# Optimization experiments

Measured on AMD Instinct MI355X. Metric: run time of the kernel, lower is better.

The kernel has to match this reference:

```python
import jax, jax.numpy as jnp
import numpy as np

N_LAYERS = 4
D_MODEL = 256
P = 128            # ssm_size // 2 (conj_sym S5)
LATENT_DIM = 256
MAX_SEQ_LEN = 32768
OUTPUT_DIM = 64
LN_EPS = 1e-6      # flax nn.LayerNorm default


def layer_norm(x, scale, bias):
    mu = jnp.mean(x, axis=-1, keepdims=True)
    var = jnp.mean(jnp.square(x - mu), axis=-1, keepdims=True)
    return (x - mu) * jax.lax.rsqrt(var + LN_EPS) * scale + bias


def s5_ssm(u, Lre, Lim, Bre, Bim, Cre, Cim, Dvec, log_step, resets):
    """u: (L, H) float. Returns (L, H) float. conj_sym S5, zoh discretization."""
    step = jnp.exp(log_step)                       # (P,)
    Lam = Lre + 1j * Lim                           # (P,) complex
    Lam_bar = jnp.exp(Lam * step)                  # (P,)
    B_bar = ((Lam_bar - 1.0) / Lam)[:, None] * (Bre + 1j * Bim)  # (P, H)
    Bu = u @ B_bar.T                               # (L, P) complex
    A = jnp.broadcast_to(Lam_bar, Bu.shape)        # (L, P)
    c = resets[:, None].astype(u.dtype)            # (L, 1)

    def binop(qi, qj):
        Ai, bi, ci = qi
        Aj, bj, cj = qj
        return (Aj * Ai * (1.0 - cj) + Aj * cj,
                (Aj * bi + bj) * (1.0 - cj) + bj * cj,
                ci * (1.0 - cj) + cj)

    # zero initial hidden state => no prepend needed (identical result)
    _, xs, _ = jax.lax.associative_scan(binop, (A, Bu, c))
    y = 2.0 * jnp.real(xs @ (Cre + 1j * Cim).T)    # (L, H), conj_sym doubling
    return y + u * Dvec


def setup_inputs() -> dict:
    key = jax.random.key(0)
    ks = jax.random.split(key, 16)
    f = jax.random.normal
    return {
        "latent": f(ks[0], (LATENT_DIM,), jnp.float32),
        "W_expand": f(ks[1], (LATENT_DIM, D_MODEL), jnp.float32) / np.sqrt(LATENT_DIM),
        "b_expand": jnp.zeros((D_MODEL,), jnp.float32),
        "norm_scale": jnp.ones((N_LAYERS, D_MODEL), jnp.float32),
        "norm_bias": jnp.zeros((N_LAYERS, D_MODEL), jnp.float32),
        "Lambda_re": -(0.1 + 0.9 * jax.random.uniform(ks[2], (N_LAYERS, P))),
        "Lambda_im": np.pi * f(ks[3], (N_LAYERS, P), jnp.float32),
        "B_re": f(ks[4], (N_LAYERS, P, D_MODEL), jnp.float32) / np.sqrt(D_MODEL),
        "B_im": f(ks[5], (N_LAYERS, P, D_MODEL), jnp.float32) / np.sqrt(D_MODEL),
        "C_re": f(ks[6], (N_LAYERS, D_MODEL, P), jnp.float32) / np.sqrt(P),
        "C_im": f(ks[7], (N_LAYERS, D_MODEL, P), jnp.float32) / np.sqrt(P),
        "D": f(ks[8], (N_LAYERS, D_MODEL), jnp.float32),
        "log_step": jnp.log(jax.random.uniform(ks[9], (N_LAYERS, P), minval=1e-3, maxval=1e-1)),
        "W1": f(ks[10], (N_LAYERS, D_MODEL, D_MODEL), jnp.float32) / np.sqrt(D_MODEL),
        "b1": jnp.zeros((N_LAYERS, D_MODEL), jnp.float32),
        "W2": f(ks[11], (N_LAYERS, D_MODEL, D_MODEL), jnp.float32) / np.sqrt(D_MODEL),
        "b2": jnp.zeros((N_LAYERS, D_MODEL), jnp.float32),
        "W_out": f(ks[12], (D_MODEL, OUTPUT_DIM), jnp.float32) / np.sqrt(D_MODEL),
        "b_out": jnp.zeros((OUTPUT_DIM,), jnp.float32),
        "seq_len": MAX_SEQ_LEN,
    }


def reference(latent, W_expand, b_expand, norm_scale, norm_bias,
              Lambda_re, Lambda_im, B_re, B_im, C_re, C_im, D, log_step,
              W1, b1, W2, b2, W_out, b_out, seq_len):
    # latent_expand + leaky_relu, then broadcast to full trajectory
    x = jax.nn.leaky_relu(latent @ W_expand + b_expand)        # (H,)
    x = jnp.broadcast_to(x[None, :], (MAX_SEQ_LEN, D_MODEL))    # (L, H); batch dim of 1 dropped
    resets = jnp.zeros((MAX_SEQ_LEN,), x.dtype)                 # dones = zeros
    for i in range(N_LAYERS):
        skip = x
        h = layer_norm(x, norm_scale[i], norm_bias[i])          # prenorm
        y = s5_ssm(h, Lambda_re[i], Lambda_im[i], B_re[i], B_im[i],
                   C_re[i], C_im[i], D[i], log_step[i], resets)
        y = layer_norm(y, norm_scale[i], norm_bias[i])          # gtrxl norm (shared params)
        y = jax.nn.gelu(y)
        y = (y @ W1[i] + b1[i]) * jax.nn.sigmoid(y @ W2[i] + b2[i])  # full_glu
        x = skip + y
    return x @ W_out + b_out                                    # (L, output_dim)
```

## Files before the change

### kernel.cpp

```cpp
#include <hip/hip_runtime.h>
#include <stdint.h>

#define LSEQ 32768
#define NCH 512
#define TCH 64

typedef _Float16 half8 __attribute__((ext_vector_type(8)));
typedef _Float16 half4v __attribute__((ext_vector_type(4)));
typedef _Float16 half2v __attribute__((ext_vector_type(2)));
typedef float f32x4 __attribute__((ext_vector_type(4)));
typedef float f32x2 __attribute__((ext_vector_type(2)));

__device__ __forceinline__ float sigmoidf_(float x) { return 1.f / (1.f + __expf(-x)); }
__device__ __forceinline__ float gelu_(float x) {
    float z = 0.7978845608028654f * (x + 0.044715f * x * x * x);
    float e = __expf(2.f * z);
    float t = 1.f - 2.f / (e + 1.f);
    return 0.5f * x * (1.f + t);
}

__device__ __forceinline__ void gll16(const _Float16* gp, _Float16* lp) {
    __builtin_amdgcn_global_load_lds((__attribute__((address_space(1))) void*)gp,
                                     (__attribute__((address_space(3))) void*)lp, 16, 0, 0);
}

__global__ __launch_bounds__(512) void s5_k0a(const float* __restrict__ lre, const float* __restrict__ lim,
                                              const float* __restrict__ lstep,
                                              float* aR, float* aI, float* cbR, float* cbI,
                                              float* aTR, float* aTI, float* alp, float* ralp) {
    int i = threadIdx.x;
    float st = expf(lstep[i]);
    float lr = lre[i] * st, li = lim[i] * st;
    float ea = expf(lr);
    float ar = ea * cosf(li), ai = ea * sinf(li);
    float den = lre[i] * lre[i] + lim[i] * lim[i];
    float nr = ar - 1.f, ni = ai;
    float cr = (nr * lre[i] + ni * lim[i]) / den;
    float ci = (ni * lre[i] - nr * lim[i]) / den;
    float cm = sqrtf(cr * cr + ci * ci);
    float al = sqrtf(2.83f / fmaxf(cm, 1e-8f));
    float eT = expf(lr * (float)TCH);
    aR[i] = ar; aI[i] = ai;
    cbR[i] = cr; cbI[i] = ci;
    aTR[i] = eT * cosf(li * (float)TCH);
    aTI[i] = eT * sinf(li * (float)TCH);
    alp[i] = al; ralp[i] = 1.f / al;
}

__global__ __launch_bounds__(256) void s5_k0b(const float* __restrict__ Bre, const float* __restrict__ Bim,
                                              const float* __restrict__ Cre, const float* __restrict__ Cim,
                                              const float* __restrict__ W1, const float* __restrict__ W2,
                                              const float* __restrict__ b1, const float* __restrict__ b2,
                                              const float* __restrict__ Wout,
                                              const float* __restrict__ cbR, const float* __restrict__ cbI,
                                              const float* __restrict__ alp, const float* __restrict__ ralp,
                                              _Float16* Wbu, _Float16* Wc, _Float16* Wglu,
                                              _Float16* WoutT, float* bglu) {
    int stride = gridDim.x * blockDim.x;
    int tid0 = blockIdx.x * blockDim.x + threadIdx.x;
    for (int i = tid0; i < 262144; i += stride) {
        int l = i >> 16, n = (i >> 8) & 255, k = i & 255;
        int s = n >> 4, lmn = n & 15;
        int p = l * 128 + (s >> 1) * 16 + lmn;
        float re = cbR[p] * Bre[p * 256 + k] - cbI[p] * Bim[p * 256 + k];
        float im = cbR[p] * Bim[p * 256 + k] + cbI[p] * Bre[p * 256 + k];
        Wbu[i] = (_Float16)(((s & 1) ? im : re) * alp[p]);
    }
    for (int i = tid0; i < 262144; i += stride) {
        int l = i >> 16, n = (i >> 8) & 255, k = i & 255;
        int p = k >> 1;
        float base = (k & 1) ? -2.f * Cim[(l * 256 + n) * 128 + p]
                             : 2.f * Cre[(l * 256 + n) * 128 + p];
        Wc[i] = (_Float16)(base * ralp[l * 128 + p]);
    }
    for (int i = tid0; i < 524288; i += stride) {
        int l = i >> 17, n = (i >> 8) & 511, k = i & 255;
        int j = ((n >> 7) << 6) | (((n >> 6) & 1) << 5) | (((n >> 5) & 1) << 4) | (n & 15);
        const float* src = ((n >> 4) & 1) ? W2 : W1;
        Wglu[i] = (_Float16)src[(l * 256 + k) * 256 + j];
    }
    for (int i = tid0; i < 16384; i += stride) {
        int n = i >> 8, k = i & 255;
        WoutT[i] = (_Float16)Wout[k * 64 + n];
    }
    for (int i = tid0; i < 2048; i += stride) {
        int l = i >> 9, n = i & 511;
        int j = ((n >> 7) << 6) | (((n >> 6) & 1) << 5) | (((n >> 5) & 1) << 4) | (n & 15);
        bglu[i] = (((n >> 4) & 1) ? b2 : b1)[l * 256 + j];
    }
}

__global__ __launch_bounds__(256) void s5_k0c(const float* __restrict__ latent, const float* __restrict__ W,
                                              const float* __restrict__ b, _Float16* __restrict__ x0h) {
    __shared__ float lat[256];
    lat[threadIdx.x] = latent[threadIdx.x];
    __syncthreads();
    float s = b[threadIdx.x];
    for (int k = 0; k < 256; ++k) s += lat[k] * W[k * 256 + threadIdx.x];
    x0h[threadIdx.x] = (_Float16)((s > 0.f) ? s : 0.01f * s);
}

__global__ __launch_bounds__(256) void s5_k1_fill(const _Float16* __restrict__ x0h, _Float16* __restrict__ x) {
    int i = blockIdx.x * 256 + threadIdx.x;
    half8 v = *(const half8*)(x0h + (i & 31) * 8);
    *(half8*)(x + i * 8) = v;
}

__global__ __launch_bounds__(512, 1) void s5_k3_lngemm(const _Float16* __restrict__ x,
                                                       const _Float16* __restrict__ Wt,
                                                       const float* __restrict__ gamma,
                                                       const float* __restrict__ beta,
                                                       _Float16* __restrict__ h,
                                                       _Float16* __restrict__ Buh) {
    __shared__ _Float16 sW[128 * 512];
    int tid = threadIdx.x, wid = tid >> 6, lane = tid & 63;
    int lm = lane & 15, quad = lane >> 4;
    int m0 = blockIdx.x * 128;
    int rowb = m0 + wid * 16;

#pragma unroll
    for (int half = 0; half < 2; ++half)
#pragma unroll
        for (int i = 0; i < 8; ++i) {
            int c = i * 8 + wid;
            int ks = c >> 3, n16 = c & 7;
            gll16(Wt + (half * 128 + n16 * 16 + lm) * 256 + ks * 32 + quad * 8,
                  sW + half * 32768 + c * 512);
        }

    int row = rowb + lm;
    half8 af[8];
    {
        half8 xv[8];
#pragma unroll
        for (int ks = 0; ks < 8; ++ks)
            xv[ks] = *(const half8*)(x + row * 256 + ks * 32 + quad * 8);
        float s1 = 0.f, s2 = 0.f;
#pragma unroll
        for (int i = 0; i < 8; ++i)
#pragma unroll
            for (int j = 0; j < 8; ++j) { float t = (float)xv[i][j]; s1 += t; s2 += t * t; }
        s1 += __shfl_xor(s1, 16, 64); s2 += __shfl_xor(s2, 16, 64);
        s1 += __shfl_xor(s1, 32, 64); s2 += __shfl_xor(s2, 32, 64);
        float mu = s1 * (1.f / 256.f);
        float var = s2 * (1.f / 256.f) - mu * mu;
        float rs = rsqrtf(fmaxf(var, 0.f) + 1e-6f);
#pragma unroll
        for (int ks = 0; ks < 8; ++ks) {
            f32x4 g0 = *(const f32x4*)(gamma + ks * 32 + quad * 8);
            f32x4 g1 = *(const f32x4*)(gamma + ks * 32 + quad * 8 + 4);
            f32x4 b0 = *(const f32x4*)(beta + ks * 32 + quad * 8);
            f32x4 b1 = *(const f32x4*)(beta + ks * 32 + quad * 8 + 4);
            half8 o;
#pragma unroll
            for (int j = 0; j < 4; ++j) {
                o[j]     = (_Float16)(((float)xv[ks][j] - mu) * rs * g0[j] + b0[j]);
                o[j + 4] = (_Float16)(((float)xv[ks][j + 4] - mu) * rs * g1[j] + b1[j]);
            }
            af[ks] = o;
            *(half8*)(h + row * 256 + ks * 32 + quad * 8) = o;
        }
    }
    asm volatile("s_waitcnt vmcnt(0)" ::: "memory");
    __syncthreads();

    f32x4 zero = {0.f, 0.f, 0.f, 0.f};
    f32x4 acc[2][8];
#pragma unroll
    for (int hf = 0; hf < 2; ++hf)
#pragma unroll
        for (int nt = 0; nt < 8; ++nt) acc[hf][nt] = zero;

#pragma unroll
    for (int hf = 0; hf < 2; ++hf)
#pragma unroll
        for (int ks = 0; ks < 8; ++ks) {
            half8 bf[8];
#pragma unroll
            for (int nt = 0; nt < 8; ++nt)
                bf[nt] = *(const half8*)(sW + hf * 32768 + (ks * 8 + nt) * 512 + lane * 8);
#pragma unroll
            for (int nt = 0; nt < 8; ++nt)
                acc[hf][nt] = __builtin_amdgcn_mfma_f32_16x16x32_f16(af[ks], bf[nt], acc[hf][nt], 0, 0, 0);
        }

#pragma unroll
    for (int u = 0; u < 8; ++u) {
        int hf = u >> 2, q = u & 3;
        int p = u * 16 + lm;
#pragma unroll
        for (int r = 0; r < 4; ++r) {
            half2v o = {(_Float16)acc[hf][2 * q][r], (_Float16)acc[hf][2 * q + 1][r]};
            *(half2v*)(Buh + (rowb + quad * 4 + r) * 256 + 2 * p) = o;
        }
    }
}

__global__ __launch_bounds__(128, 4) void s5_k4_carry(const _Float16* __restrict__ Bu,
                                                      const float* __restrict__ aR, const float* __restrict__ aI,
                                                      float* __restrict__ carRI) {
    int p = threadIdx.x, c = blockIdx.x;
    int t0 = c * TCH;
    const _Float16* bp = Bu + t0 * 256 + 2 * p;
    half2v hv[TCH];
#pragma unroll
    for (int j = 0; j < TCH; ++j) hv[j] = *(const half2v*)(bp + j * 256);
    float ar = aR[p], ai = aI[p];
    float sr = 0.f, si = 0.f;
#pragma unroll
    for (int j = 0; j < TCH; ++j) {
        float nr = fmaf(ar, sr, fmaf(-ai, si, (float)hv[j][0]));
        float ni = fmaf(ar, si, fmaf(ai, sr, (float)hv[j][1]));
        sr = nr; si = ni;
    }
    *(f32x2*)(carRI + (c * 128 + p) * 2) = f32x2{sr, si};
}

__global__ __launch_bounds__(512, 1) void s5_k7_gemm_c(const _Float16* __restrict__ Bu,
                                                       const float* __restrict__ carRI,
                                                       const _Float16* __restrict__ Wt,
                                                       const _Float16* __restrict__ h,
                                                       const float* __restrict__ aR, const float* __restrict__ aI,
                                                       const float* __restrict__ aTR, const float* __restrict__ aTI,
                                                       const float* __restrict__ Dv,
                                                       const float* __restrict__ gamma,
                                                       const float* __restrict__ beta,
                                                       _Float16* __restrict__ g) {
    __shared__ _Float16 sW[64 * 512];
    __shared__ _Float16 xsT[128 * 256];
    int tid = threadIdx.x, wid = tid >> 6, lane = tid & 63;
    int lm = lane & 15, quad = lane >> 4;
    int m0 = blockIdx.x * 128;
    int rowb = m0 + wid * 16;

    auto stageW = [&](int half) {
#pragma unroll
        for (int i = 0; i < 8; ++i) {
            int c = i * 8 + wid;
            int ks = c >> 3, n16 = c & 7;
            gll16(Wt + (half * 128 + n16 * 16 + lm) * 256 + ks * 32 + quad * 8, sW + c * 512);
        }
    };
    stageW(0);

    if (tid < 256) {
        int cc = tid >> 7, p = tid & 127;
        int cg = blockIdx.x * 2 + cc;
        const _Float16* bp = Bu + (m0 + cc * TCH) * 256 + 2 * p;
        half2v hv[TCH];
#pragma unroll
        for (int j = 0; j < TCH; ++j) hv[j] = *(const half2v*)(bp + j * 256);
        float tr = aTR[p], ti = aTI[p];
        float cr = 0.f, ci = 0.f;
#pragma unroll 8
        for (int i = 0; i < cg; ++i) {
            f32x2 w = *(const f32x2*)(carRI + (i * 128 + p) * 2);
            float nr = fmaf(tr, cr, fmaf(-ti, ci, w[0]));
            float ni = fmaf(tr, ci, fmaf(ti, cr, w[1]));
            cr = nr; ci = ni;
        }
        float ar = aR[p], ai = aI[p];
        float sr = cr, si = ci;
#pragma unroll
        for (int j = 0; j < TCH; ++j) {
            float nr = fmaf(ar, sr, fmaf(-ai, si, (float)hv[j][0]));
            float ni = fmaf(ar, si, fmaf(ai, sr, (float)hv[j][1]));
            sr = nr; si = ni;
            int rl = cc * TCH + j;
            int byte = (4 * p) ^ ((rl & 7) << 4);
            *(half2v*)((char*)xsT + rl * 512 + byte) = half2v{(_Float16)sr, (_Float16)si};
        }
    }
    asm volatile("s_waitcnt vmcnt(0)" ::: "memory");
    __syncthreads();

    int rl = wid * 16 + lm;
    half8 af[8];
#pragma unroll
    for (int ks = 0; ks < 8; ++ks) {
        int b = ks * 64 + quad * 16;
        af[ks] = *(const half8*)((const char*)xsT + rl * 512 + (b ^ ((rl & 7) << 4)));
    }

    f32x4 zero = {0.f, 0.f, 0.f, 0.f};
    f32x4 acc[2][8];
#pragma unroll
    for (int hf = 0; hf < 2; ++hf)
#pragma unroll
        for (int nt = 0; nt < 8; ++nt) acc[hf][nt] = zero;

#pragma unroll
    for (int ks = 0; ks < 8; ++ks) {
        half8 bf[8];
#pragma unroll
        for (int nt = 0; nt < 8; ++nt)
            bf[nt] = *(const half8*)(sW + (ks * 8 + nt) * 512 + lane * 8);
#pragma unroll
        for (int nt = 0; nt < 8; ++nt)
            acc[0][nt] = __builtin_amdgcn_mfma_f32_16x16x32_f16(af[ks], bf[nt], acc[0][nt], 0, 0, 0);
    }
    __syncthreads();
    stageW(1);
    asm volatile("s_waitcnt vmcnt(0)" ::: "memory");
    __syncthreads();
#pragma unroll
    for (int ks = 0; ks < 8; ++ks) {
        half8 bf[8];
#pragma unroll
        for (int nt = 0; nt < 8; ++nt)
            bf[nt] = *(const half8*)(sW + (ks * 8 + nt) * 512 + lane * 8);
#pragma unroll
        for (int nt = 0; nt < 8; ++nt)
            acc[1][nt] = __builtin_amdgcn_mfma_f32_16x16x32_f16(af[ks], bf[nt], acc[1][nt], 0, 0, 0);
    }

#pragma unroll
    for (int hf = 0; hf < 2; ++hf)
#pragma unroll
        for (int nt = 0; nt < 8; ++nt) {
            int col = hf * 128 + nt * 16 + lm;
            float dv = Dv[col];
#pragma unroll
            for (int r = 0; r < 4; ++r)
                acc[hf][nt][r] += (float)h[(rowb + quad * 4 + r) * 256 + col] * dv;
        }
    float mu[4], rs[4];
#pragma unroll
    for (int r = 0; r < 4; ++r) {
        float a = 0.f, b = 0.f;
#pragma unroll
        for (int hf = 0; hf < 2; ++hf)
#pragma unroll
            for (int nt = 0; nt < 8; ++nt) {
                float v = acc[hf][nt][r];
                a += v; b += v * v;
            }
#pragma unroll
        for (int off = 1; off < 16; off <<= 1) {
            a += __shfl_xor(a, off, 64);
            b += __shfl_xor(b, off, 64);
        }
        float m = a * (1.f / 256.f);
        float var = b * (1.f / 256.f) - m * m;
        mu[r] = m;
        rs[r] = rsqrtf(fmaxf(var, 0.f) + 1e-6f);
    }
#pragma unroll
    for (int hf = 0; hf < 2; ++hf)
#pragma unroll
        for (int nt = 0; nt < 8; ++nt) {
            int col = hf * 128 + nt * 16 + lm;
            float ga = gamma[col], be = beta[col];
#pragma unroll
            for (int r = 0; r < 4; ++r) {
                float hn = (acc[hf][nt][r] - mu[r]) * rs[r] * ga + be;
                g[(rowb + quad * 4 + r) * 256 + col] = (_Float16)gelu_(hn);
            }
        }
}

__global__ __launch_bounds__(256, 2) void s5_k8_gemm_glu(const _Float16* __restrict__ A,
                                                         const _Float16* __restrict__ Wt,
                                                         const float* __restrict__ bias,
                                                         _Float16* __restrict__ x) {
    __shared__ _Float16 sW[64 * 512];
    int tid = threadIdx.x, wid = tid >> 6, lane = tid & 63;
    int lm = lane & 15, quad = lane >> 4;
    int n0 = blockIdx.y * 128;
    int m0 = blockIdx.x * 128;
#pragma unroll
    for (int i = 0; i < 16; ++i) {
        int c = i * 4 + wid;
        int ks = c >> 3, n16 = c & 7;
        gll16(Wt + (n0 + n16 * 16 + lm) * 256 + ks * 32 + quad * 8, sW + c * 512);
    }
    int rowb = m0 + wid * 32;
    half8 af[2][8];
#pragma unroll
    for (int mt = 0; mt < 2; ++mt)
#pragma unroll
        for (int ks = 0; ks < 8; ++ks)
            af[mt][ks] = *(const half8*)(A + (rowb + mt * 16 + lm) * 256 + ks * 32 + quad * 8);
    asm volatile("s_waitcnt vmcnt(0)" ::: "memory");
    __syncthreads();

    f32x4 zero = {0.f, 0.f, 0.f, 0.f};
    f32x4 acc[2][8];
#pragma unroll
    for (int mt = 0; mt < 2; ++mt)
#pragma unroll
        for (int nt = 0; nt < 8; ++nt) acc[mt][nt] = zero;
#pragma unroll
    for (int ks = 0; ks < 8; ++ks) {
        half8 bf[8];
#pragma unroll
        for (int nt = 0; nt < 8; ++nt)
            bf[nt] = *(const half8*)(sW + (ks * 8 + nt) * 512 + lane * 8);
#pragma unroll
        for (int mt = 0; mt < 2; ++mt)
#pragma unroll
            for (int nt = 0; nt < 8; ++nt)
                acc[mt][nt] = __builtin_amdgcn_mfma_f32_16x16x32_f16(af[mt][ks], bf[nt], acc[mt][nt], 0, 0, 0);
    }
    int jbase = (n0 >> 1) + lm;
    _Float16 xold[2][4][4];
#pragma unroll
    for (int mt = 0; mt < 2; ++mt)
#pragma unroll
        for (int q = 0; q < 4; ++q)
#pragma unroll
            for (int r = 0; r < 4; ++r)
                xold[mt][q][r] = x[(rowb + mt * 16 + quad * 4 + r) * 256 + jbase + q * 16];
#pragma unroll
    for (int mt = 0; mt < 2; ++mt)
#pragma unroll
        for (int q = 0; q < 4; ++q) {
            float b1v = bias[n0 + (2 * q) * 16 + lm];
            float b2v = bias[n0 + (2 * q + 1) * 16 + lm];
            int jcol = jbase + q * 16;
#pragma unroll
            for (int r = 0; r < 4; ++r) {
                float u1 = acc[mt][2 * q][r] + b1v;
                float u2 = acc[mt][2 * q + 1][r] + b2v;
                float gl = u1 * sigmoidf_(u2);
                int idx = (rowb + mt * 16 + quad * 4 + r) * 256 + jcol;
                x[idx] = (_Float16)((float)xold[mt][q][r] + gl);
            }
        }
}

__global__ __launch_bounds__(256, 2) void s5_k9_gemm_out(const _Float16* __restrict__ A,
                                                         const _Float16* __restrict__ Wt,
                                                         const float* __restrict__ bout,
                                                         float* __restrict__ out) {
    __shared__ _Float16 sW[32 * 512];
    int tid = threadIdx.x, wid = tid >> 6, lane = tid & 63;
    int lm = lane & 15, quad = lane >> 4;
    int m0 = blockIdx.x * 128;
#pragma unroll
    for (int i = 0; i < 8; ++i) {
        int c = i * 4 + wid;
        int ks = c >> 2, n16 = c & 3;
        gll16(Wt + (n16 * 16 + lm) * 256 + ks * 32 + quad * 8, sW + c * 512);
    }
    int rowb = m0 + wid * 32;
    half8 af[2][8];
#pragma unroll
    for (int mt = 0; mt < 2; ++mt)
#pragma unroll
        for (int ks = 0; ks < 8; ++ks)
            af[mt][ks] = *(const half8*)(A + (rowb + mt * 16 + lm) * 256 + ks * 32 + quad * 8);
    asm volatile("s_waitcnt vmcnt(0)" ::: "memory");
    __syncthreads();

    f32x4 zero = {0.f, 0.f, 0.f, 0.f};
    f32x4 acc[2][4];
#pragma unroll
    for (int mt = 0; mt < 2; ++mt)
#pragma unroll
        for (int nt = 0; nt < 4; ++nt) acc[mt][nt] = zero;
#pragma unroll
    for (int ks = 0; ks < 8; ++ks) {
        half8 bf[4];
#pragma unroll
        for (int nt = 0; nt < 4; ++nt)
            bf[nt] = *(const half8*)(sW + (ks * 4 + nt) * 512 + lane * 8);
#pragma unroll
        for (int mt = 0; mt < 2; ++mt)
#pragma unroll
            for (int nt = 0; nt < 4; ++nt)
                acc[mt][nt] = __builtin_amdgcn_mfma_f32_16x16x32_f16(af[mt][ks], bf[nt], acc[mt][nt], 0, 0, 0);
    }
#pragma unroll
    for (int mt = 0; mt < 2; ++mt)
#pragma unroll
        for (int nt = 0; nt < 4; ++nt) {
            int col = nt * 16 + lm;
            float bv = bout[col];
#pragma unroll
            for (int r = 0; r < 4; ++r) {
                int row = rowb + mt * 16 + quad * 4 + r;
                out[row * 64 + col] = acc[mt][nt][r] + bv;
            }
        }
}

constexpr size_t OFF_X    = 0;
constexpr size_t OFF_BU   = 33554432;
constexpr size_t OFF_H    = 67108864;
constexpr size_t OFF_WBU  = 100663296;
constexpr size_t OFF_WC   = OFF_WBU + 524288;
constexpr size_t OFF_WGLU = OFF_WC + 524288;
constexpr size_t OFF_WOUT = OFF_WGLU + 1048576;
constexpr size_t OFF_BGLU = OFF_WOUT + 32768;
constexpr size_t OFF_AR   = OFF_BGLU + 8192;
constexpr size_t OFF_AI   = OFF_AR + 2048;
constexpr size_t OFF_CBR  = OFF_AI + 2048;
constexpr size_t OFF_CBI  = OFF_CBR + 2048;
constexpr size_t OFF_ATR  = OFF_CBI + 2048;
constexpr size_t OFF_ATI  = OFF_ATR + 2048;
constexpr size_t OFF_ALP  = OFF_ATI + 2048;
constexpr size_t OFF_RALP = OFF_ALP + 2048;
constexpr size_t OFF_X0H  = OFF_RALP + 2048;
constexpr size_t OFF_CARRI= OFF_X0H + 1024;

extern "C" void kernel_launch(void* const* d_in, const int* in_sizes, int n_in,
                              void* d_out, int out_size, void* d_ws, size_t ws_size,
                              hipStream_t stream) {
    (void)in_sizes; (void)n_in; (void)out_size; (void)ws_size;
    const float* latent    = (const float*)d_in[0];
    const float* W_expand  = (const float*)d_in[1];
    const float* b_expand  = (const float*)d_in[2];
    const float* norm_s    = (const float*)d_in[3];
    const float* norm_b    = (const float*)d_in[4];
    const float* Lre       = (const float*)d_in[5];
    const float* Lim       = (const float*)d_in[6];
    const float* Bre       = (const float*)d_in[7];
    const float* Bim       = (const float*)d_in[8];
    const float* Cre       = (const float*)d_in[9];
    const float* Cim       = (const float*)d_in[10];
    const float* Dv        = (const float*)d_in[11];
    const float* lstep     = (const float*)d_in[12];
    const float* W1        = (const float*)d_in[13];
    const float* b1        = (const float*)d_in[14];
    const float* W2        = (const float*)d_in[15];
    const float* b2        = (const float*)d_in[16];
    const float* Wout      = (const float*)d_in[17];
    const float* bout      = (const float*)d_in[18];

    char* ws = (char*)d_ws;
    _Float16* x    = (_Float16*)(ws + OFF_X);
    _Float16* Buh  = (_Float16*)(ws + OFF_BU);
    _Float16* gbuf = (_Float16*)(ws + OFF_BU + 16777216);
    _Float16* hbuf = (_Float16*)(ws + OFF_H);
    _Float16* Wbu  = (_Float16*)(ws + OFF_WBU);
    _Float16* Wc   = (_Float16*)(ws + OFF_WC);
    _Float16* Wglu = (_Float16*)(ws + OFF_WGLU);
    _Float16* WoutT= (_Float16*)(ws + OFF_WOUT);
    float* bglu = (float*)(ws + OFF_BGLU);
    float* aR  = (float*)(ws + OFF_AR);
    float* aI  = (float*)(ws + OFF_AI);
    float* cbR = (float*)(ws + OFF_CBR);
    float* cbI = (float*)(ws + OFF_CBI);
    float* aTR = (float*)(ws + OFF_ATR);
    float* aTI = (float*)(ws + OFF_ATI);
    float* alp = (float*)(ws + OFF_ALP);
    float* ralp= (float*)(ws + OFF_RALP);
    _Float16* x0h = (_Float16*)(ws + OFF_X0H);
    float* carRI=(float*)(ws + OFF_CARRI);

    s5_k0a<<<1, 512, 0, stream>>>(Lre, Lim, lstep, aR, aI, cbR, cbI, aTR, aTI, alp, ralp);
    s5_k0b<<<256, 256, 0, stream>>>(Bre, Bim, Cre, Cim, W1, W2, b1, b2, Wout,
                                    cbR, cbI, alp, ralp, Wbu, Wc, Wglu, WoutT, bglu);
    s5_k0c<<<1, 256, 0, stream>>>(latent, W_expand, b_expand, x0h);
    s5_k1_fill<<<4096, 256, 0, stream>>>(x0h, x);

    for (int l = 0; l < 4; ++l) {
        s5_k3_lngemm<<<256, 512, 0, stream>>>(x, Wbu + l * 65536,
                                              norm_s + l * 256, norm_b + l * 256,
                                              hbuf, Buh);
        s5_k4_carry<<<NCH, 128, 0, stream>>>(Buh, aR + l * 128, aI + l * 128, carRI);
        s5_k7_gemm_c<<<256, 512, 0, stream>>>(Buh, carRI, Wc + l * 65536, hbuf,
                                              aR + l * 128, aI + l * 128,
                                              aTR + l * 128, aTI + l * 128,
                                              Dv + l * 256,
                                              norm_s + l * 256, norm_b + l * 256, gbuf);
        s5_k8_gemm_glu<<<dim3(256, 4), 256, 0, stream>>>(gbuf, Wglu + l * 131072,
                                                         bglu + l * 512, x);
    }
    s5_k9_gemm_out<<<256, 256, 0, stream>>>(x, WoutT, bout, (float*)d_out);
}
```

Before: 477.3 us.

## Fuse C-projection/LN/GELU kernel with GLU GEMM via shared-memory staging

Merges the C-projection + layernorm + GELU kernel and the GLU GEMM into one kernel per layer. The GELU output stays in a swizzled shared-memory tile instead of going through a global buffer, and the four GLU weight column blocks are staged one after another into the same shared-memory region. This removes a 16 MB global write and read per layer and one launch. In exchange the GLU work loses its separate 256x4 grid parallelism, and each weight stage is serialized with syncs inside one 512-thread block.

```diff
diff --git a/kernel.cpp b/kernel.cpp
--- a/kernel.cpp
+++ b/kernel.cpp
@@ -216,16 +216,18 @@
     *(f32x2*)(carRI + (c * 128 + p) * 2) = f32x2{sr, si};
 }
 
-__global__ __launch_bounds__(512, 1) void s5_k7_gemm_c(const _Float16* __restrict__ Bu,
-                                                       const float* __restrict__ carRI,
-                                                       const _Float16* __restrict__ Wt,
-                                                       const _Float16* __restrict__ h,
-                                                       const float* __restrict__ aR, const float* __restrict__ aI,
-                                                       const float* __restrict__ aTR, const float* __restrict__ aTI,
-                                                       const float* __restrict__ Dv,
-                                                       const float* __restrict__ gamma,
-                                                       const float* __restrict__ beta,
-                                                       _Float16* __restrict__ g) {
+__global__ __launch_bounds__(512, 1) void s5_k7_mega(const _Float16* __restrict__ Bu,
+                                                     const float* __restrict__ carRI,
+                                                     const _Float16* __restrict__ Wc,
+                                                     const _Float16* __restrict__ Wglu,
+                                                     const _Float16* __restrict__ h,
+                                                     const float* __restrict__ aR, const float* __restrict__ aI,
+                                                     const float* __restrict__ aTR, const float* __restrict__ aTI,
+                                                     const float* __restrict__ Dv,
+                                                     const float* __restrict__ gamma,
+                                                     const float* __restrict__ beta,
+                                                     const float* __restrict__ bias,
+                                                     _Float16* __restrict__ x) {
     __shared__ _Float16 sW[64 * 512];
     __shared__ _Float16 xsT[128 * 256];
     int tid = threadIdx.x, wid = tid >> 6, lane = tid & 63;
@@ -233,15 +235,23 @@
     int m0 = blockIdx.x * 128;
     int rowb = m0 + wid * 16;
 
-    auto stageW = [&](int half) {
+    auto stageWc = [&](int half) {
 #pragma unroll
         for (int i = 0; i < 8; ++i) {
             int c = i * 8 + wid;
             int ks = c >> 3, n16 = c & 7;
-            gll16(Wt + (half * 128 + n16 * 16 + lm) * 256 + ks * 32 + quad * 8, sW + c * 512);
+            gll16(Wc + (half * 128 + n16 * 16 + lm) * 256 + ks * 32 + quad * 8, sW + c * 512);
         }
     };
-    stageW(0);
+    auto stageWg = [&](int n0) {
+#pragma unroll
+        for (int i = 0; i < 8; ++i) {
+            int c = i * 8 + wid;
+            int ks = c >> 3, n16 = c & 7;
+            gll16(Wglu + (n0 + n16 * 16 + lm) * 256 + ks * 32 + quad * 8, sW + c * 512);
+        }
+    };
+    stageWc(0);
 
     if (tid < 256) {
         int cc = tid >> 7, p = tid & 127;
@@ -300,7 +310,7 @@
             acc[0][nt] = __builtin_amdgcn_mfma_f32_16x16x32_f16(af[ks], bf[nt], acc[0][nt], 0, 0, 0);
     }
     __syncthreads();
-    stageW(1);
+    stageWc(1);
     asm volatile("s_waitcnt vmcnt(0)" ::: "memory");
     __syncthreads();
 #pragma unroll
@@ -354,65 +364,45 @@
 #pragma unroll
             for (int r = 0; r < 4; ++r) {
                 float hn = (acc[hf][nt][r] - mu[r]) * rs[r] * ga + be;
-                g[(rowb + quad * 4 + r) * 256 + col] = (_Float16)gelu_(hn);
+                int rg = wid * 16 + quad * 4 + r;
+                int byte = (2 * col) ^ ((rg & 7) << 4);
+                *((_Float16*)((char*)xsT + rg * 512 + byte)) = (_Float16)gelu_(hn);
             }
         }
-}
-
-__global__ __launch_bounds__(256, 2) void s5_k8_gemm_glu(const _Float16* __restrict__ A,
-                                                         const _Float16* __restrict__ Wt,
-                                                         const float* __restrict__ bias,
-                                                         _Float16* __restrict__ x) {
-    __shared__ _Float16 sW[64 * 512];
-    int tid = threadIdx.x, wid = tid >> 6, lane = tid & 63;
-    int lm = lane & 15, quad = lane >> 4;
-    int n0 = blockIdx.y * 128;
-    int m0 = blockIdx.x * 128;
-#pragma unroll
-    for (int i = 0; i < 16; ++i) {
-        int c = i * 4 + wid;
-        int ks = c >> 3, n16 = c & 7;
-        gll16(Wt + (n0 + n16 * 16 + lm) * 256 + ks * 32 + quad * 8, sW + c * 512);
-    }
-    int rowb = m0 + wid * 32;
-    half8 af[2][8];
-#pragma unroll
-    for (int mt = 0; mt < 2; ++mt)
-#pragma unroll
-        for (int ks = 0; ks < 8; ++ks)
-            af[mt][ks] = *(const half8*)(A + (rowb + mt * 16 + lm) * 256 + ks * 32 + quad * 8);
+    __syncthreads();
+    stageWg(0);
+    half8 ag[8];
+#pragma unroll
+    for (int ks = 0; ks < 8; ++ks) {
+        int b = ks * 64 + quad * 16;
+        ag[ks] = *(const half8*)((const char*)xsT + rl * 512 + (b ^ ((rl & 7) << 4)));
+    }
     asm volatile("s_waitcnt vmcnt(0)" ::: "memory");
     __syncthreads();
 
-    f32x4 zero = {0.f, 0.f, 0.f, 0.f};
-    f32x4 acc[2][8];
-#pragma unroll
-    for (int mt = 0; mt < 2; ++mt)
-#pragma unroll
-        for (int nt = 0; nt < 8; ++nt) acc[mt][nt] = zero;
-#pragma unroll
-    for (int ks = 0; ks < 8; ++ks) {
-        half8 bf[8];
-#pragma unroll
-        for (int nt = 0; nt < 8; ++nt)
-            bf[nt] = *(const half8*)(sW + (ks * 8 + nt) * 512 + lane * 8);
-#pragma unroll
-        for (int mt = 0; mt < 2; ++mt)
+#pragma unroll
+    for (int cy = 0; cy < 4; ++cy) {
+        f32x4 accg[8];
+#pragma unroll
+        for (int nt = 0; nt < 8; ++nt) accg[nt] = zero;
+#pragma unroll
+        for (int ks = 0; ks < 8; ++ks) {
+            half8 bf[8];
 #pragma unroll
             for (int nt = 0; nt < 8; ++nt)
-                acc[mt][nt] = __builtin_amdgcn_mfma_f32_16x16x32_f16(af[mt][ks], bf[nt], acc[mt][nt], 0, 0, 0);
-    }
-    int jbase = (n0 >> 1) + lm;
-    _Float16 xold[2][4][4];
-#pragma unroll
-    for (int mt = 0; mt < 2; ++mt)
+                bf[nt] = *(const half8*)(sW + (ks * 8 + nt) * 512 + lane * 8);
+#pragma unroll
+            for (int nt = 0; nt < 8; ++nt)
+                accg[nt] = __builtin_amdgcn_mfma_f32_16x16x32_f16(ag[ks], bf[nt], accg[nt], 0, 0, 0);
+        }
+        int n0 = cy * 128;
+        int jbase = (n0 >> 1) + lm;
+        _Float16 xold[4][4];
 #pragma unroll
         for (int q = 0; q < 4; ++q)
 #pragma unroll
             for (int r = 0; r < 4; ++r)
-                xold[mt][q][r] = x[(rowb + mt * 16 + quad * 4 + r) * 256 + jbase + q * 16];
-#pragma unroll
-    for (int mt = 0; mt < 2; ++mt)
+                xold[q][r] = x[(rowb + quad * 4 + r) * 256 + jbase + q * 16];
 #pragma unroll
         for (int q = 0; q < 4; ++q) {
             float b1v = bias[n0 + (2 * q) * 16 + lm];
@@ -420,13 +410,20 @@
             int jcol = jbase + q * 16;
 #pragma unroll
             for (int r = 0; r < 4; ++r) {
-                float u1 = acc[mt][2 * q][r] + b1v;
-                float u2 = acc[mt][2 * q + 1][r] + b2v;
+                float u1 = accg[2 * q][r] + b1v;
+                float u2 = accg[2 * q + 1][r] + b2v;
                 float gl = u1 * sigmoidf_(u2);
-                int idx = (rowb + mt * 16 + quad * 4 + r) * 256 + jcol;
-                x[idx] = (_Float16)((float)xold[mt][q][r] + gl);
+                int idx = (rowb + quad * 4 + r) * 256 + jcol;
+                x[idx] = (_Float16)((float)xold[q][r] + gl);
             }
         }
+        if (cy < 3) {
+            __syncthreads();
+            stageWg((cy + 1) * 128);
+            asm volatile("s_waitcnt vmcnt(0)" ::: "memory");
+            __syncthreads();
+        }
+    }
 }
 
 __global__ __launch_bounds__(256, 2) void s5_k9_gemm_out(const _Float16* __restrict__ A,
@@ -531,7 +528,6 @@
     char* ws = (char*)d_ws;
     _Float16* x    = (_Float16*)(ws + OFF_X);
     _Float16* Buh  = (_Float16*)(ws + OFF_BU);
-    _Float16* gbuf = (_Float16*)(ws + OFF_BU + 16777216);
     _Float16* hbuf = (_Float16*)(ws + OFF_H);
     _Float16* Wbu  = (_Float16*)(ws + OFF_WBU);
     _Float16* Wc   = (_Float16*)(ws + OFF_WC);
@@ -560,13 +556,13 @@
                                               norm_s + l * 256, norm_b + l * 256,
                                               hbuf, Buh);
         s5_k4_carry<<<NCH, 128, 0, stream>>>(Buh, aR + l * 128, aI + l * 128, carRI);
-        s5_k7_gemm_c<<<256, 512, 0, stream>>>(Buh, carRI, Wc + l * 65536, hbuf,
-                                              aR + l * 128, aI + l * 128,
-                                              aTR + l * 128, aTI + l * 128,
-                                              Dv + l * 256,
-                                              norm_s + l * 256, norm_b + l * 256, gbuf);
-        s5_k8_gemm_glu<<<dim3(256, 4), 256, 0, stream>>>(gbuf, Wglu + l * 131072,
-                                                         bglu + l * 512, x);
+        s5_k7_mega<<<256, 512, 0, stream>>>(Buh, carRI, Wc + l * 65536, Wglu + l * 131072,
+                                            hbuf,
+                                            aR + l * 128, aI + l * 128,
+                                            aTR + l * 128, aTI + l * 128,
+                                            Dv + l * 256,
+                                            norm_s + l * 256, norm_b + l * 256,
+                                            bglu + l * 512, x);
     }
     s5_k9_gemm_out<<<256, 256, 0, stream>>>(x, WoutT, bout, (float*)d_out);
 }
```

Measured after the change: 461.1 us. 1.04x faster.
